# Kernel tuning notes

Hardware: AMD Instinct MI355X
Metric: run time of the kernel (lower is better)

Reference implementation:

```python
import jax, jax.numpy as jnp
import numpy as np

N_NODES = 100000
N_EDGES = 1600000
H_FEATS = 64


def setup_inputs() -> dict:
    key = jax.random.key(0)
    k_h, k_src, k_dst, k_w1, k_b1, k_w2, k_b2 = jax.random.split(key, 7)
    h = jax.random.normal(k_h, (N_NODES, H_FEATS), dtype=jnp.float32)
    src = jax.random.randint(k_src, (N_EDGES,), 0, N_NODES, dtype=jnp.int64)
    dst = jax.random.randint(k_dst, (N_EDGES,), 0, N_NODES, dtype=jnp.int64)
    # Linear params (torch Linear: y = x @ W.T + b). Store as [in, out] for jnp.
    lim1 = 1.0 / np.sqrt(2 * H_FEATS)
    W1 = jax.random.uniform(k_w1, (2 * H_FEATS, H_FEATS), minval=-lim1, maxval=lim1, dtype=jnp.float32)
    b1 = jax.random.uniform(k_b1, (H_FEATS,), minval=-lim1, maxval=lim1, dtype=jnp.float32)
    lim2 = 1.0 / np.sqrt(H_FEATS)
    W2 = jax.random.uniform(k_w2, (H_FEATS, 1), minval=-lim2, maxval=lim2, dtype=jnp.float32)
    b2 = jax.random.uniform(k_b2, (1,), minval=-lim2, maxval=lim2, dtype=jnp.float32)
    return {"h": h, "src": src, "dst": dst, "W1": W1, "b1": b1, "W2": W2, "b2": b2}


def reference(h, src, dst, W1, b1, W2, b2):
    # Gather src/dst node features per edge, avoid materializing the concat by
    # splitting W1 into the src-half and dst-half of the contraction.
    W1s, W1d = W1[:H_FEATS], W1[H_FEATS:]            # each [h, h]
    h_src = h[src]                                    # [E, h]
    h_dst = h[dst]                                    # [E, h]
    hidden = jax.nn.relu(h_src @ W1s + h_dst @ W1d + b1)  # [E, h]
    score = (hidden @ W2 + b2)[:, 0]                  # [E]
    return score
```

## Files before the change

kernel.cpp:

```cpp
#include <hip/hip_runtime.h>
#include <hip/hip_fp16.h>


#define HF  64
#define TN  64
#define PAD 68

__global__ __launch_bounds__(512) void node_proj_kernel(
    const float* __restrict__ h, const float* __restrict__ W1,
    const float* __restrict__ b1, __half* __restrict__ P,
    __half* __restrict__ Q, int n_nodes)
{
    __shared__ float hs[TN * PAD];

    const int tid  = threadIdx.x;
    const int lane = tid & 63;
    const int wave = __builtin_amdgcn_readfirstlane(tid >> 6);
    const int c0   = wave * 16;
    const bool isQ = c0 >= 64;
    const int ccol = c0 & 63;

    const float* wbase = W1 + (isQ ? (HF * HF) : 0) + ccol;
    __half* const outh = (isQ ? Q : P) + ccol;

    const int n0   = blockIdx.x * TN;
    const int nrow = (n_nodes - n0 < TN) ? (n_nodes - n0) : TN;

    {
        const int maxf4 = nrow * 16;
        const float4* hv = (const float4*)(h + (size_t)n0 * HF);
        #pragma unroll
        for (int it = 0; it < 2; ++it) {
            const int idx  = tid + it * 512;
            const int cidx = (idx < maxf4) ? idx : 0;
            const float4 v = hv[cidx];
            const int row = idx >> 4;
            const int c4  = (idx & 15) * 4;
            *(float4*)&hs[row * PAD + c4] = v;
        }
    }
    __syncthreads();

    float hreg[64];
    {
        const float* r = &hs[lane * PAD];
        #pragma unroll
        for (int k4 = 0; k4 < 16; ++k4) {
            const float4 v = *(const float4*)(r + k4 * 4);
            hreg[k4 * 4 + 0] = v.x;
            hreg[k4 * 4 + 1] = v.y;
            hreg[k4 * 4 + 2] = v.z;
            hreg[k4 * 4 + 3] = v.w;
        }
    }

    float acc[16];
    #pragma unroll
    for (int j = 0; j < 16; ++j) acc[j] = isQ ? 0.0f : b1[ccol + j];

    #pragma unroll
    for (int k = 0; k < 64; ++k) {
        const float a = hreg[k];
        const float* w = wbase + k * HF;
        #pragma unroll
        for (int j = 0; j < 16; ++j)
            acc[j] = fmaf(a, w[j], acc[j]);
    }

    if (lane < nrow) {
        union { uint4 u[2]; __half2 hh[8]; } pk;
        #pragma unroll
        for (int j = 0; j < 8; ++j)
            pk.hh[j] = __floats2half2_rn(acc[2 * j], acc[2 * j + 1]);
        __half* base = outh + (size_t)(n0 + lane) * HF;
        *(uint4*)(base)     = pk.u[0];
        *(uint4*)(base + 8) = pk.u[1];
    }
}

__device__ __forceinline__ float dot8_relu(uint4 pv, uint4 qv, float4 wa, float4 wb) {
    const __half2* ph = (const __half2*)&pv;
    const __half2* qh = (const __half2*)&qv;
    const float2 p0 = __half22float2(ph[0]), q0 = __half22float2(qh[0]);
    const float2 p1 = __half22float2(ph[1]), q1 = __half22float2(qh[1]);
    const float2 p2 = __half22float2(ph[2]), q2 = __half22float2(qh[2]);
    const float2 p3 = __half22float2(ph[3]), q3 = __half22float2(qh[3]);
    float acc = 0.f;
    acc = fmaf(fmaxf(p0.x + q0.x, 0.f), wa.x, acc);
    acc = fmaf(fmaxf(p0.y + q0.y, 0.f), wa.y, acc);
    acc = fmaf(fmaxf(p1.x + q1.x, 0.f), wa.z, acc);
    acc = fmaf(fmaxf(p1.y + q1.y, 0.f), wa.w, acc);
    acc = fmaf(fmaxf(p2.x + q2.x, 0.f), wb.x, acc);
    acc = fmaf(fmaxf(p2.y + q2.y, 0.f), wb.y, acc);
    acc = fmaf(fmaxf(p3.x + q3.x, 0.f), wb.z, acc);
    acc = fmaf(fmaxf(p3.y + q3.y, 0.f), wb.w, acc);
    return acc;
}

__device__ __forceinline__ float red8(float v) {
    v += __shfl_xor(v, 4, 8);
    v += __shfl_xor(v, 2, 8);
    v += __shfl_xor(v, 1, 8);
    return v;
}

__global__ __launch_bounds__(256) void edge_score_kernel(
    const __half* __restrict__ P, const __half* __restrict__ Q,
    const int* __restrict__ src, const int* __restrict__ dst,
    const float* __restrict__ W2, const float* __restrict__ b2,
    float* __restrict__ out, int n_edges)
{
    const int tid   = blockIdx.x * 256 + threadIdx.x;
    const int sub   = threadIdx.x & 7;
    const int group = tid >> 3;
    const int j0    = sub * 8;
    const int e0    = group * 8;
    if (e0 >= n_edges) return;

    const float4 w2a = *(const float4*)(W2 + j0);
    const float4 w2b = *(const float4*)(W2 + j0 + 4);
    const float bias2 = b2[0];

    if (e0 + 8 <= n_edges) {
        const int4 sA = *(const int4*)(src + e0);
        const int4 sB = *(const int4*)(src + e0 + 4);
        const int4 dA = *(const int4*)(dst + e0);
        const int4 dB = *(const int4*)(dst + e0 + 4);

        const uint4 p0 = *(const uint4*)(P + (size_t)sA.x * HF + j0);
        const uint4 p1 = *(const uint4*)(P + (size_t)sA.y * HF + j0);
        const uint4 p2 = *(const uint4*)(P + (size_t)sA.z * HF + j0);
        const uint4 p3 = *(const uint4*)(P + (size_t)sA.w * HF + j0);
        const uint4 p4 = *(const uint4*)(P + (size_t)sB.x * HF + j0);
        const uint4 p5 = *(const uint4*)(P + (size_t)sB.y * HF + j0);
        const uint4 p6 = *(const uint4*)(P + (size_t)sB.z * HF + j0);
        const uint4 p7 = *(const uint4*)(P + (size_t)sB.w * HF + j0);
        const uint4 q0 = *(const uint4*)(Q + (size_t)dA.x * HF + j0);
        const uint4 q1 = *(const uint4*)(Q + (size_t)dA.y * HF + j0);
        const uint4 q2 = *(const uint4*)(Q + (size_t)dA.z * HF + j0);
        const uint4 q3 = *(const uint4*)(Q + (size_t)dA.w * HF + j0);
        const uint4 q4 = *(const uint4*)(Q + (size_t)dB.x * HF + j0);
        const uint4 q5 = *(const uint4*)(Q + (size_t)dB.y * HF + j0);
        const uint4 q6 = *(const uint4*)(Q + (size_t)dB.z * HF + j0);
        const uint4 q7 = *(const uint4*)(Q + (size_t)dB.w * HF + j0);

        float s0 = red8(dot8_relu(p0, q0, w2a, w2b));
        float s1 = red8(dot8_relu(p1, q1, w2a, w2b));
        float s2 = red8(dot8_relu(p2, q2, w2a, w2b));
        float s3 = red8(dot8_relu(p3, q3, w2a, w2b));
        float s4 = red8(dot8_relu(p4, q4, w2a, w2b));
        float s5 = red8(dot8_relu(p5, q5, w2a, w2b));
        float s6 = red8(dot8_relu(p6, q6, w2a, w2b));
        float s7 = red8(dot8_relu(p7, q7, w2a, w2b));

        if (sub == 0) {
            *(float4*)(out + e0)     = make_float4(s0 + bias2, s1 + bias2,
                                                   s2 + bias2, s3 + bias2);
            *(float4*)(out + e0 + 4) = make_float4(s4 + bias2, s5 + bias2,
                                                   s6 + bias2, s7 + bias2);
        }
    } else {
        for (int e = e0; e < n_edges; ++e) {
            const int s = src[e];
            const int d = dst[e];
            const uint4 pv = *(const uint4*)(P + (size_t)s * HF + j0);
            const uint4 qv = *(const uint4*)(Q + (size_t)d * HF + j0);
            float sc = red8(dot8_relu(pv, qv, w2a, w2b));
            if (sub == 0) out[e] = sc + bias2;
        }
    }
}

extern "C" void kernel_launch(void* const* d_in, const int* in_sizes, int n_in,
                              void* d_out, int out_size, void* d_ws, size_t ws_size,
                              hipStream_t stream) {
    const float* h   = (const float*)d_in[0];
    const int*   src = (const int*)d_in[1];
    const int*   dst = (const int*)d_in[2];
    const float* W1  = (const float*)d_in[3];
    const float* b1  = (const float*)d_in[4];
    const float* W2  = (const float*)d_in[5];
    const float* b2  = (const float*)d_in[6];
    float* out = (float*)d_out;

    const int n_nodes = in_sizes[0] / HF;
    const int n_edges = in_sizes[1];

    __half* P = (__half*)d_ws;
    __half* Q = P + (size_t)n_nodes * HF;

    const int nblocks1 = (n_nodes + TN - 1) / TN;
    node_proj_kernel<<<nblocks1, 512, 0, stream>>>(h, W1, b1, P, Q, n_nodes);

    const int ngroups  = (n_edges + 7) / 8;
    const int nblocks2 = (ngroups + 31) / 32;
    edge_score_kernel<<<nblocks2, 256, 0, stream>>>(P, Q, src, dst, W2, b2, out, n_edges);
}
```

Baseline: 160.6 us.

## Compute node projection with bf16 MFMA and stage output through shared memory

Replaces the per-thread FP32 FMA loop of the node projection with MFMA 16x16x32 bf16 instructions, converting h and W1 to bf16 fragments in registers. The output tile is staged through LDS as half and written with coalesced 16-byte stores to P and Q, and the block shrinks to 256 threads. This targets the compute-bound node GEMM, but every block re-reads and converts all of W1, and the bf16 inputs lose precision compared with the FP32 path. The edge kernel, which likely dominates total time, is unchanged.

```diff
diff --git a/kernel.cpp b/kernel.cpp
--- a/kernel.cpp
+++ b/kernel.cpp
@@ -3,78 +3,107 @@
 
 
 #define HF  64
-#define TN  64
-#define PAD 68
-
-__global__ __launch_bounds__(512) void node_proj_kernel(
+#define PADF 68
+#define PADH 136
+
+typedef __attribute__((ext_vector_type(8))) short bf16x8;
+typedef __attribute__((ext_vector_type(4))) float f32x4;
+
+__device__ __forceinline__ short f2bf(float x) {
+    unsigned u = __builtin_bit_cast(unsigned, x);
+    unsigned r = (u + 0x7fffu + ((u >> 16) & 1u)) >> 16;
+    return (short)r;
+}
+
+__global__ __launch_bounds__(256) void node_proj_kernel(
     const float* __restrict__ h, const float* __restrict__ W1,
     const float* __restrict__ b1, __half* __restrict__ P,
     __half* __restrict__ Q, int n_nodes)
 {
-    __shared__ float hs[TN * PAD];
+    __shared__ float hs[64 * PADF];
 
     const int tid  = threadIdx.x;
+    const int wave = tid >> 6;
     const int lane = tid & 63;
-    const int wave = __builtin_amdgcn_readfirstlane(tid >> 6);
-    const int c0   = wave * 16;
-    const bool isQ = c0 >= 64;
-    const int ccol = c0 & 63;
-
-    const float* wbase = W1 + (isQ ? (HF * HF) : 0) + ccol;
-    __half* const outh = (isQ ? Q : P) + ccol;
-
-    const int n0   = blockIdx.x * TN;
-    const int nrow = (n_nodes - n0 < TN) ? (n_nodes - n0) : TN;
+    const int q    = lane >> 4;
+    const int n    = lane & 15;
+
+    const int n0   = blockIdx.x * 64;
+    const int nrow = (n_nodes - n0 < 64) ? (n_nodes - n0) : 64;
 
     {
         const int maxf4 = nrow * 16;
         const float4* hv = (const float4*)(h + (size_t)n0 * HF);
         #pragma unroll
-        for (int it = 0; it < 2; ++it) {
-            const int idx  = tid + it * 512;
+        for (int it = 0; it < 4; ++it) {
+            const int idx  = tid + it * 256;
             const int cidx = (idx < maxf4) ? idx : 0;
             const float4 v = hv[cidx];
             const int row = idx >> 4;
             const int c4  = (idx & 15) * 4;
-            *(float4*)&hs[row * PAD + c4] = v;
-        }
-    }
+            *(float4*)&hs[row * PADF + c4] = v;
+        }
+    }
+
+    bf16x8 bfrag[8][2];
+    #pragma unroll
+    for (int t = 0; t < 8; ++t) {
+        const float* wb = W1 + ((t >= 4) ? HF * HF : 0) + (t & 3) * 16 + n;
+        #pragma unroll
+        for (int kb = 0; kb < 2; ++kb) {
+            #pragma unroll
+            for (int j = 0; j < 8; ++j)
+                bfrag[t][kb][j] = f2bf(wb[(kb * 32 + q * 8 + j) * HF]);
+        }
+    }
+
     __syncthreads();
 
-    float hreg[64];
+    bf16x8 afrag[2];
     {
-        const float* r = &hs[lane * PAD];
-        #pragma unroll
-        for (int k4 = 0; k4 < 16; ++k4) {
-            const float4 v = *(const float4*)(r + k4 * 4);
-            hreg[k4 * 4 + 0] = v.x;
-            hreg[k4 * 4 + 1] = v.y;
-            hreg[k4 * 4 + 2] = v.z;
-            hreg[k4 * 4 + 3] = v.w;
-        }
-    }
-
-    float acc[16];
-    #pragma unroll
-    for (int j = 0; j < 16; ++j) acc[j] = isQ ? 0.0f : b1[ccol + j];
-
-    #pragma unroll
-    for (int k = 0; k < 64; ++k) {
-        const float a = hreg[k];
-        const float* w = wbase + k * HF;
-        #pragma unroll
-        for (int j = 0; j < 16; ++j)
-            acc[j] = fmaf(a, w[j], acc[j]);
-    }
-
-    if (lane < nrow) {
-        union { uint4 u[2]; __half2 hh[8]; } pk;
-        #pragma unroll
-        for (int j = 0; j < 8; ++j)
-            pk.hh[j] = __floats2half2_rn(acc[2 * j], acc[2 * j + 1]);
-        __half* base = outh + (size_t)(n0 + lane) * HF;
-        *(uint4*)(base)     = pk.u[0];
-        *(uint4*)(base + 8) = pk.u[1];
+        const float* r = &hs[(wave * 16 + n) * PADF];
+        #pragma unroll
+        for (int kb = 0; kb < 2; ++kb) {
+            const float* rk = r + kb * 32 + q * 8;
+            #pragma unroll
+            for (int j = 0; j < 8; ++j) afrag[kb][j] = f2bf(rk[j]);
+        }
+    }
+
+    f32x4 acc[8];
+    #pragma unroll
+    for (int t = 0; t < 8; ++t) {
+        acc[t] = (f32x4){0.f, 0.f, 0.f, 0.f};
+        acc[t] = __builtin_amdgcn_mfma_f32_16x16x32_bf16(afrag[0], bfrag[t][0], acc[t], 0, 0, 0);
+        acc[t] = __builtin_amdgcn_mfma_f32_16x16x32_bf16(afrag[1], bfrag[t][1], acc[t], 0, 0, 0);
+    }
+
+    __syncthreads();
+
+    __half* hs2 = (__half*)hs;
+    #pragma unroll
+    for (int t = 0; t < 8; ++t) {
+        const float bb = (t < 4) ? b1[(t & 3) * 16 + n] : 0.0f;
+        #pragma unroll
+        for (int r = 0; r < 4; ++r) {
+            const int row = wave * 16 + q * 4 + r;
+            hs2[row * PADH + t * 16 + n] = __float2half(acc[t][r] + bb);
+        }
+    }
+    __syncthreads();
+
+    #pragma unroll
+    for (int it = 0; it < 4; ++it) {
+        const int idx  = tid + it * 256;
+        const int row  = idx >> 4;
+        const int part = idx & 15;
+        if (row < nrow) {
+            const uint4 v = *(const uint4*)&hs2[row * PADH + part * 8];
+            __half* dstp = (part < 8)
+                ? (P + (size_t)(n0 + row) * HF + part * 8)
+                : (Q + (size_t)(n0 + row) * HF + (part - 8) * 8);
+            *(uint4*)dstp = v;
+        }
     }
 }
 
@@ -189,8 +218,8 @@
     __half* P = (__half*)d_ws;
     __half* Q = P + (size_t)n_nodes * HF;
 
-    const int nblocks1 = (n_nodes + TN - 1) / TN;
-    node_proj_kernel<<<nblocks1, 512, 0, stream>>>(h, W1, b1, P, Q, n_nodes);
+    const int nblocks1 = (n_nodes + 63) / 64;
+    node_proj_kernel<<<nblocks1, 256, 0, stream>>>(h, W1, b1, P, Q, n_nodes);
 
     const int ngroups  = (n_edges + 7) / 8;
     const int nblocks2 = (ngroups + 31) / 32;
```

After: 149.7 us. 6.8% less time.
